# Optimization experiments

Measured on AMD Instinct MI355X. Metric: run time of the kernel, lower is better.

The kernel has to match this reference:

```python
import jax, jax.numpy as jnp
import numpy as np

BATCH, SEQ_LEN, NUM_TAGS = 1024, 512, 48


def setup_inputs() -> dict:
    key = jax.random.key(0)
    k1, k2 = jax.random.split(key)
    potentials = jax.random.normal(k1, (BATCH, SEQ_LEN, NUM_TAGS), dtype=jnp.float32)
    transition_params = jax.random.normal(k2, (NUM_TAGS, NUM_TAGS), dtype=jnp.float32)
    return {"potentials": potentials, "transition_params": transition_params}


def reference(potentials, transition_params):
    """Viterbi forward decode for a linear-chain CRF.

    potentials: [B, T, num_tags] unary potentials.
    transition_params: [num_tags, num_tags] binary potentials.
    Returns:
      backpointers: [B, T-1, num_tags] int32 argmax backpointers.
      scores: [B, num_tags] final Viterbi scores.
    """
    init_state = potentials[:, 0]                 # [B, num_tags]
    rest = jnp.swapaxes(potentials[:, 1:], 0, 1)  # [T-1, B, num_tags]

    def step(state, inputs):
        # state: [B, num_tags]; inputs: [B, num_tags]
        # transition_scores[b, i, j] = state[b, i] + trans[i, j]
        transition_scores = state[:, :, None] + transition_params[None]  # [B, tags, tags]
        new_state = inputs + jnp.max(transition_scores, axis=1)          # [B, tags]
        backpointers = jnp.argmax(transition_scores, axis=1).astype(jnp.int32)
        return new_state, backpointers

    final_state, backpointers = jax.lax.scan(step, init_state, rest)
    backpointers = jnp.swapaxes(backpointers, 0, 1)  # [B, T-1, num_tags]
    return backpointers, final_state
```

## Files before the change

### kernel.cpp

```cpp
#include <hip/hip_runtime.h>


constexpr int B_ = 1024;
constexpr int T_ = 512;
constexpr int K_ = 48;
constexpr int C_ = 6;

__global__ __launch_bounds__(64, 1) void crf_viterbi_kernel(
    const float* __restrict__ pot,
    const float* __restrict__ trans,
    float* __restrict__ out)
{
    const int b = blockIdx.x;
    const int j = threadIdx.x;

    __shared__ __align__(16) float stv[K_];

    float tcol[K_];
    #pragma unroll
    for (int i = 0; i < K_; ++i) tcol[i] = trans[i * K_ + j];

    const float* pp = pot + (size_t)b * T_ * K_ + j;
    float* bpp      = out + (size_t)b * (T_ - 1) * K_ + j;
    float* scout    = out + (size_t)B_ * (T_ - 1) * K_ + (size_t)b * K_ + j;

    float myst = pp[0];
    stv[j] = myst;
    __builtin_amdgcn_wave_barrier();

    float cand_prev[K_];
    float mm_prev = 0.0f;

    auto step = [&](float pcur, bool do_shadow) {
        float4 sv[12];
        const float4* stv4 = (const float4*)stv;
        #pragma unroll
        for (int c = 0; c < 12; ++c) sv[c] = stv4[c];

        if (do_shadow) {
            int xx = K_ - 1;
            #pragma unroll
            for (int i = K_ - 2; i >= 0; --i)
                xx = (cand_prev[i] == mm_prev) ? i : xx;
            *bpp = (float)xx;
            bpp += K_;
        }

        #pragma unroll
        for (int c = 0; c < 12; ++c) {
            cand_prev[4 * c + 0] = sv[c].x + tcol[4 * c + 0];
            cand_prev[4 * c + 1] = sv[c].y + tcol[4 * c + 1];
            cand_prev[4 * c + 2] = sv[c].z + tcol[4 * c + 2];
            cand_prev[4 * c + 3] = sv[c].w + tcol[4 * c + 3];
        }

        float m[24];
        #pragma unroll
        for (int p = 0; p < 24; ++p) m[p] = fmaxf(cand_prev[2 * p], cand_prev[2 * p + 1]);
        #pragma unroll
        for (int p = 0; p < 12; ++p) m[p] = fmaxf(m[2 * p], m[2 * p + 1]);
        #pragma unroll
        for (int p = 0; p < 6; ++p)  m[p] = fmaxf(m[2 * p], m[2 * p + 1]);
        #pragma unroll
        for (int p = 0; p < 3; ++p)  m[p] = fmaxf(m[2 * p], m[2 * p + 1]);
        float mm = fmaxf(fmaxf(m[0], m[1]), m[2]);
        mm_prev = mm;

        myst = pcur + mm;
        stv[j] = myst;
        __builtin_amdgcn_wave_barrier();
    };

    float p1 = pp[(size_t)1 * K_];
    float pbuf[C_];
    #pragma unroll
    for (int u = 0; u < C_; ++u) pbuf[u] = pp[(size_t)(2 + u) * K_];

    step(p1, false);

    for (int t0 = 2; t0 < T_; t0 += C_) {
        float pc[C_];
        #pragma unroll
        for (int u = 0; u < C_; ++u) pc[u] = pbuf[u];

        #pragma unroll
        for (int u = 0; u < C_; ++u) {
            int tn = t0 + C_ + u;
            if (tn > T_ - 1) tn = T_ - 1;
            pbuf[u] = pp[(size_t)tn * K_];
        }

        #pragma unroll
        for (int u = 0; u < C_; ++u) step(pc[u], true);
    }

    {
        int xx = K_ - 1;
        #pragma unroll
        for (int i = K_ - 2; i >= 0; --i)
            xx = (cand_prev[i] == mm_prev) ? i : xx;
        *bpp = (float)xx;
    }

    *scout = myst;
}

extern "C" void kernel_launch(void* const* d_in, const int* in_sizes, int n_in,
                              void* d_out, int out_size, void* d_ws, size_t ws_size,
                              hipStream_t stream) {
    const float* pot   = (const float*)d_in[0];
    const float* trans = (const float*)d_in[1];
    float* out         = (float*)d_out;
    crf_viterbi_kernel<<<dim3(B_), dim3(K_), 0, stream>>>(pot, trans, out);
}
```

Baseline: 322.9 us.

## Split Viterbi into serial state pass and parallel backpointer recompute pass

```diff
diff --git a/kernel.cpp b/kernel.cpp
--- a/kernel.cpp
+++ b/kernel.cpp
@@ -4,9 +4,8 @@
 constexpr int B_ = 1024;
 constexpr int T_ = 512;
 constexpr int K_ = 48;
-constexpr int C_ = 6;
 
-__global__ __launch_bounds__(64, 1) void crf_viterbi_kernel(
+__global__ __launch_bounds__(64, 1) void crf_state_kernel(
     const float* __restrict__ pot,
     const float* __restrict__ trans,
     float* __restrict__ out)
@@ -21,88 +20,124 @@
     for (int i = 0; i < K_; ++i) tcol[i] = trans[i * K_ + j];
 
     const float* pp = pot + (size_t)b * T_ * K_ + j;
-    float* bpp      = out + (size_t)b * (T_ - 1) * K_ + j;
+    float* stout    = out + ((size_t)b * (T_ - 1) + 1) * K_ + j;
     float* scout    = out + (size_t)B_ * (T_ - 1) * K_ + (size_t)b * K_ + j;
 
     float myst = pp[0];
     stv[j] = myst;
     __builtin_amdgcn_wave_barrier();
 
-    float cand_prev[K_];
-    float mm_prev = 0.0f;
-
-    auto step = [&](float pcur, bool do_shadow) {
+    auto step = [&](float pcur, bool do_store) {
         float4 sv[12];
         const float4* stv4 = (const float4*)stv;
         #pragma unroll
         for (int c = 0; c < 12; ++c) sv[c] = stv4[c];
+        __builtin_amdgcn_wave_barrier();
 
-        if (do_shadow) {
-            int xx = K_ - 1;
-            #pragma unroll
-            for (int i = K_ - 2; i >= 0; --i)
-                xx = (cand_prev[i] == mm_prev) ? i : xx;
-            *bpp = (float)xx;
-            bpp += K_;
-        }
-
+        float cand[K_];
         #pragma unroll
         for (int c = 0; c < 12; ++c) {
-            cand_prev[4 * c + 0] = sv[c].x + tcol[4 * c + 0];
-            cand_prev[4 * c + 1] = sv[c].y + tcol[4 * c + 1];
-            cand_prev[4 * c + 2] = sv[c].z + tcol[4 * c + 2];
-            cand_prev[4 * c + 3] = sv[c].w + tcol[4 * c + 3];
+            cand[4 * c + 0] = sv[c].x + tcol[4 * c + 0];
+            cand[4 * c + 1] = sv[c].y + tcol[4 * c + 1];
+            cand[4 * c + 2] = sv[c].z + tcol[4 * c + 2];
+            cand[4 * c + 3] = sv[c].w + tcol[4 * c + 3];
         }
-
-        float m[24];
+        float m1[16];
         #pragma unroll
-        for (int p = 0; p < 24; ++p) m[p] = fmaxf(cand_prev[2 * p], cand_prev[2 * p + 1]);
+        for (int k = 0; k < 16; ++k)
+            m1[k] = fmaxf(fmaxf(cand[3 * k], cand[3 * k + 1]), cand[3 * k + 2]);
+        float m2[6];
         #pragma unroll
-        for (int p = 0; p < 12; ++p) m[p] = fmaxf(m[2 * p], m[2 * p + 1]);
-        #pragma unroll
-        for (int p = 0; p < 6; ++p)  m[p] = fmaxf(m[2 * p], m[2 * p + 1]);
-        #pragma unroll
-        for (int p = 0; p < 3; ++p)  m[p] = fmaxf(m[2 * p], m[2 * p + 1]);
-        float mm = fmaxf(fmaxf(m[0], m[1]), m[2]);
-        mm_prev = mm;
+        for (int k = 0; k < 5; ++k)
+            m2[k] = fmaxf(fmaxf(m1[3 * k], m1[3 * k + 1]), m1[3 * k + 2]);
+        m2[5] = m1[15];
+        float mm = fmaxf(fmaxf(fmaxf(m2[0], m2[1]), m2[2]),
+                         fmaxf(fmaxf(m2[3], m2[4]), m2[5]));
 
         myst = pcur + mm;
         stv[j] = myst;
         __builtin_amdgcn_wave_barrier();
+
+        if (do_store) { *stout = myst; stout += K_; }
     };
 
     float p1 = pp[(size_t)1 * K_];
-    float pbuf[C_];
+    float pbuf[6];
     #pragma unroll
-    for (int u = 0; u < C_; ++u) pbuf[u] = pp[(size_t)(2 + u) * K_];
+    for (int u = 0; u < 6; ++u) pbuf[u] = pp[(size_t)(2 + u) * K_];
 
-    step(p1, false);
+    step(p1, true);
 
-    for (int t0 = 2; t0 < T_; t0 += C_) {
-        float pc[C_];
+    for (int t0 = 2; t0 <= 500; t0 += 6) {
+        float pc[6];
         #pragma unroll
-        for (int u = 0; u < C_; ++u) pc[u] = pbuf[u];
+        for (int u = 0; u < 6; ++u) pc[u] = pbuf[u];
+        #pragma unroll
+        for (int u = 0; u < 6; ++u) pbuf[u] = pp[(size_t)(t0 + 6 + u) * K_];
+        #pragma unroll
+        for (int u = 0; u < 6; ++u) step(pc[u], true);
+    }
+    #pragma unroll
+    for (int u = 0; u < 5; ++u) step(pbuf[u], true);
+    step(pbuf[5], false);
 
+    *scout = myst;
+}
+
+__global__ __launch_bounds__(64, 4) void crf_bp_kernel(
+    const float* __restrict__ pot,
+    const float* __restrict__ trans,
+    float* out)
+{
+    const int s = blockIdx.x;
+    const int b = blockIdx.y;
+    const int j = threadIdx.x;
+    const int jj = j < K_ ? j : K_ - 1;
+
+    float tcol[K_];
+    #pragma unroll
+    for (int i = 0; i < K_; ++i) tcol[i] = trans[i * K_ + jj];
+
+    const int r0 = s * 64;
+    const int r1 = (r0 + 64 < T_ - 1) ? r0 + 64 : T_ - 1;
+
+    for (int r = r0; r < r1; ++r) {
+        const float* srow = out + ((size_t)b * (T_ - 1) + r) * K_;
+        if (r == 0) srow = pot + (size_t)b * T_ * K_;
+
+        float4 sv[12];
+        const float4* srow4 = (const float4*)srow;
         #pragma unroll
-        for (int u = 0; u < C_; ++u) {
-            int tn = t0 + C_ + u;
-            if (tn > T_ - 1) tn = T_ - 1;
-            pbuf[u] = pp[(size_t)tn * K_];
+        for (int c = 0; c < 12; ++c) sv[c] = srow4[c];
+
+        float cand[K_];
+        #pragma unroll
+        for (int c = 0; c < 12; ++c) {
+            cand[4 * c + 0] = sv[c].x + tcol[4 * c + 0];
+            cand[4 * c + 1] = sv[c].y + tcol[4 * c + 1];
+            cand[4 * c + 2] = sv[c].z + tcol[4 * c + 2];
+            cand[4 * c + 3] = sv[c].w + tcol[4 * c + 3];
         }
+        float m1[16];
+        #pragma unroll
+        for (int k = 0; k < 16; ++k)
+            m1[k] = fmaxf(fmaxf(cand[3 * k], cand[3 * k + 1]), cand[3 * k + 2]);
+        float m2[6];
+        #pragma unroll
+        for (int k = 0; k < 5; ++k)
+            m2[k] = fmaxf(fmaxf(m1[3 * k], m1[3 * k + 1]), m1[3 * k + 2]);
+        m2[5] = m1[15];
+        float mm = fmaxf(fmaxf(fmaxf(m2[0], m2[1]), m2[2]),
+                         fmaxf(fmaxf(m2[3], m2[4]), m2[5]));
 
-        #pragma unroll
-        for (int u = 0; u < C_; ++u) step(pc[u], true);
-    }
-
-    {
         int xx = K_ - 1;
         #pragma unroll
         for (int i = K_ - 2; i >= 0; --i)
-            xx = (cand_prev[i] == mm_prev) ? i : xx;
-        *bpp = (float)xx;
+            xx = (cand[i] == mm) ? i : xx;
+
+        if (j < K_)
+            out[((size_t)b * (T_ - 1) + r) * K_ + j] = (float)xx;
     }
-
-    *scout = myst;
 }
 
 extern "C" void kernel_launch(void* const* d_in, const int* in_sizes, int n_in,
@@ -111,5 +146,6 @@
     const float* pot   = (const float*)d_in[0];
     const float* trans = (const float*)d_in[1];
     float* out         = (float*)d_out;
-    crf_viterbi_kernel<<<dim3(B_), dim3(K_), 0, stream>>>(pot, trans, out);
+    crf_state_kernel<<<dim3(B_), dim3(K_), 0, stream>>>(pot, trans, out);
+    crf_bp_kernel<<<dim3(8, B_), dim3(64), 0, stream>>>(pot, trans, out);
 }
```

Measured after the change: 481.2 us. +49.0%, slower.
